# Kernel tuning notes

Measured on AMD Instinct MI355X. Metric: run time of the kernel, lower is better.

## Reference

```python
import jax, jax.numpy as jnp
import numpy as np

# dissected_Conv2d forward: grouped conv (groups=in_channels) producing one
# feature map per (input_channel, output_channel) pair, then permute_add_featuremaps:
# a gather by add_perm followed by a segmented sum over input channels, plus bias.

IN_C, OUT_C = 64, 64
KH, KW = 3, 3
B, H, W = 8, 56, 56
PAD = 1


def setup_inputs() -> dict:
    key = jax.random.key(0)
    k1, k2, k3 = jax.random.split(key, 3)
    x = jax.random.normal(k1, (B, IN_C, H, W), dtype=jnp.float32)
    # from_conv.weight: [out_channels, in_channels, kh, kw]
    weight = jax.random.normal(k2, (OUT_C, IN_C, KH, KW), dtype=jnp.float32) * 0.05
    bias = jax.random.normal(k3, (OUT_C,), dtype=jnp.float32) * 0.05
    return {"x": x, "weight": weight, "bias": bias}


def reference(x, weight, bias):
    out_c, in_c, kh, kw = weight.shape
    # make_preadd_conv: weight.view(in*out, 1, kh, kw)[weight_perm].
    # weight_perm maps grouped-conv channel k = i*out + j  ->  W[j, i], i.e. a
    # (out,in) -> (in,out) transpose of the leading dims.
    w_grp = jnp.transpose(weight, (1, 0, 2, 3)).reshape(in_c * out_c, 1, kh, kw)
    # grouped conv, groups = in_channels: group i convolves input channel i with
    # out_c kernels, giving preadd[:, i*out + j] = conv2d(x[:, i], W[j, i]).
    preadd = jax.lax.conv_general_dilated(
        x, w_grp,
        window_strides=(1, 1),
        padding=((PAD, PAD), (PAD, PAD)),
        dimension_numbers=("NCHW", "OIHW", "NCHW"),
        feature_group_count=in_c,
    )  # [B, in*out, H, W]
    # permute_add_featuremaps: gather with add_perm (channel p = o*in + i pulls
    # preadd channel i*out + o), then split/cat/sum == reshape [B,out,in,H,W].sum(in).
    p = jnp.arange(out_c * in_c)
    add_perm = (p % in_c) * out_c + p // in_c
    gathered = preadd[:, add_perm]  # [B, out*in, H, W]
    b_, _, h_, w_ = gathered.shape
    summed = gathered.reshape(b_, out_c, in_c, h_, w_).sum(axis=2)  # [B, out, H, W]
    # bias add: from_conv.bias.unsqueeze(1).unsqueeze(1) broadcast over H, W
    return summed + bias[None, :, None, None]
```

## Files before the change

kernel.cpp:

```cpp
#include <hip/hip_runtime.h>


typedef __attribute__((ext_vector_type(8))) short bf8_t;
typedef __attribute__((ext_vector_type(4))) float f4_t;

#define IC 64
#define OC 64
#define HH 56
#define WW 56
#define NB 8
#define NS 18
#define NPIX (HH * WW)
#define LCOLS 66
#define LDS_U16 (3 * LCOLS * 64)

__device__ __forceinline__ unsigned short f2bf(float f) {
    unsigned u = __float_as_uint(f);
    return (unsigned short)((u + 0x7FFFu + ((u >> 16) & 1u)) >> 16);
}

__global__ __launch_bounds__(256)
void repack_w(const float* __restrict__ w, unsigned short* __restrict__ wf) {
    const int s    = blockIdx.x;
    const int tid  = threadIdx.x;
    const int wv   = tid >> 6;
    const int lane = tid & 63;
    const int oc   = wv * 16 + (lane & 15);
    const int kg   = lane >> 4;
    const int tap  = s >> 1;
    const int ic0  = (s & 1) * 32 + kg * 8;
    unsigned short tmp[8];
    #pragma unroll
    for (int j = 0; j < 8; ++j)
        tmp[j] = f2bf(w[(oc * IC + ic0 + j) * 9 + tap]);
    *(uint4*)&wf[(((s * 4 + wv) * 64) + lane) * 8] = *(const uint4*)tmp;
}

__global__ __launch_bounds__(256)
void conv_fused(const float* __restrict__ x, const unsigned short* __restrict__ wf,
                const float* __restrict__ bias, float* __restrict__ out) {
    __shared__ unsigned short xl[LDS_U16];

    int bid = (int)blockIdx.x;
    bid = (bid & 7) * (NB * HH / 8) + (bid >> 3);
    const int b = bid / HH;
    const int h = bid - b * HH;

    const int tid  = threadIdx.x;
    const int wv   = tid >> 6;
    const int lane = tid & 63;
    const int kg   = lane >> 4;
    const int l15  = lane & 15;

    bf8_t afrag[NS];
    #pragma unroll
    for (int s = 0; s < NS; ++s)
        afrag[s] = *(const bf8_t*)&wf[(((s * 4 + wv) * 64) + lane) * 8];

    for (int i = tid; i < LDS_U16 / 8; i += 256)
        ((uint4*)xl)[i] = uint4{0u, 0u, 0u, 0u};
    __syncthreads();

    {
        const int ci  = lane - 1;
        const bool cok = (ci >= 0) && (ci < WW);
        #pragma unroll
        for (int i = 0; i < 6; ++i) {
            const int combo = wv + 4 * i;
            const int icb = combo / 3;
            const int r   = combo - icb * 3;
            const int hh  = h - 1 + r;
            if (cok && hh >= 0 && hh < HH) {
                const float* src = &x[((b * IC + icb * 8) * HH + hh) * WW + ci];
                bf8_t v;
                #pragma unroll
                for (int j = 0; j < 8; ++j)
                    v[j] = (short)f2bf(src[j * HH * WW]);
                const int W = r * LCOLS + lane;
                const unsigned byte = (unsigned)W * 128u +
                                      ((unsigned)(icb ^ (W & 7)) << 4);
                *(bf8_t*)((char*)xl + byte) = v;
            }
        }
    }
    __syncthreads();

    f4_t acc[4];
    #pragma unroll
    for (int t = 0; t < 4; ++t) acc[t] = 0.f;

    #pragma unroll
    for (int s = 0; s < NS; ++s) {
        const int tap = s >> 1;
        const int dh  = tap / 3;
        const int dw  = tap - dh * 3;
        const int c   = (s & 1) * 4 + kg;
        const int R0  = dh * LCOLS + dw + l15;
        const unsigned byte0 = (unsigned)R0 * 128u +
                               ((unsigned)(c ^ (R0 & 7)) << 4);
        const char* p = (const char*)xl + byte0;
        #pragma unroll
        for (int t = 0; t < 4; ++t) {
            const bf8_t bv = *(const bf8_t*)(p + t * 2048);
            acc[t] = __builtin_amdgcn_mfma_f32_16x16x32_bf16(afrag[s], bv, acc[t], 0, 0, 0);
        }
    }

    const int oc_c = wv * 16 + kg * 4;
    float bb[4];
    #pragma unroll
    for (int rr = 0; rr < 4; ++rr) bb[rr] = bias[oc_c + rr];
    #pragma unroll
    for (int t = 0; t < 4; ++t) {
        const int px = t * 16 + l15;
        if (px < WW) {
            float* o = &out[((b * OC + oc_c) * HH + h) * WW + px];
            #pragma unroll
            for (int rr = 0; rr < 4; ++rr)
                o[rr * HH * WW] = acc[t][rr] + bb[rr];
        }
    }
}

extern "C" void kernel_launch(void* const* d_in, const int* in_sizes, int n_in,
                              void* d_out, int out_size, void* d_ws, size_t ws_size,
                              hipStream_t stream) {
    const float* x    = (const float*)d_in[0];
    const float* w    = (const float*)d_in[1];
    const float* bias = (const float*)d_in[2];
    float* out        = (float*)d_out;

    unsigned short* wf = (unsigned short*)d_ws;

    hipLaunchKernelGGL(repack_w,  dim3(NS),      dim3(256), 0, stream, w, wf);
    hipLaunchKernelGGL(conv_fused, dim3(NB * HH), dim3(256), 0, stream,
                       x, wf, bias, out);
}
```

Baseline: 68.95 us.

## Split each output row into two half-row blocks and drop LDS zero-fill

```diff
diff --git a/kernel.cpp b/kernel.cpp
--- a/kernel.cpp
+++ b/kernel.cpp
@@ -11,8 +11,8 @@
 #define NB 8
 #define NS 18
 #define NPIX (HH * WW)
-#define LCOLS 66
-#define LDS_U16 (3 * LCOLS * 64)
+#define LC34 34
+#define LDS_U16 (3 * LC34 * 64)
 
 __device__ __forceinline__ unsigned short f2bf(float f) {
     unsigned u = __float_as_uint(f);
@@ -37,14 +37,16 @@
 }
 
 __global__ __launch_bounds__(256)
-void conv_fused(const float* __restrict__ x, const unsigned short* __restrict__ wf,
-                const float* __restrict__ bias, float* __restrict__ out) {
+void conv_half(const float* __restrict__ x, const unsigned short* __restrict__ wf,
+               const float* __restrict__ bias, float* __restrict__ out) {
     __shared__ unsigned short xl[LDS_U16];
 
     int bid = (int)blockIdx.x;
-    bid = (bid & 7) * (NB * HH / 8) + (bid >> 3);
-    const int b = bid / HH;
-    const int h = bid - b * HH;
+    bid = (bid & 7) * (NB * HH * 2 / 8) + (bid >> 3);
+    const int b   = bid / (HH * 2);
+    const int rem = bid - b * (HH * 2);
+    const int h   = rem >> 1;
+    const int ph  = rem & 1;
 
     const int tid  = threadIdx.x;
     const int wv   = tid >> 6;
@@ -57,68 +59,75 @@
     for (int s = 0; s < NS; ++s)
         afrag[s] = *(const bf8_t*)&wf[(((s * 4 + wv) * 64) + lane) * 8];
 
-    for (int i = tid; i < LDS_U16 / 8; i += 256)
-        ((uint4*)xl)[i] = uint4{0u, 0u, 0u, 0u};
-    __syncthreads();
+    const int half = lane >> 5;
+    const int lc   = lane & 31;
+    const int ci   = ph * 28 - 1 + lc;
+    const bool doW = (lc < 30);
+    const bool cok = doW && (ci >= 0) && (ci < WW);
 
-    {
-        const int ci  = lane - 1;
-        const bool cok = (ci >= 0) && (ci < WW);
+    float rv[3][8];
+    #pragma unroll
+    for (int i = 0; i < 3; ++i) {
+        const int c   = wv * 6 + 2 * i + half;
+        const int icb = c / 3;
+        const int r   = c - 3 * icb;
+        const int hh  = h - 1 + r;
+        const bool ok = cok && (hh >= 0) && (hh < HH);
+        const float* src = &x[((b * IC + icb * 8) * HH + hh) * WW + ci];
         #pragma unroll
-        for (int i = 0; i < 6; ++i) {
-            const int combo = wv + 4 * i;
-            const int icb = combo / 3;
-            const int r   = combo - icb * 3;
-            const int hh  = h - 1 + r;
-            if (cok && hh >= 0 && hh < HH) {
-                const float* src = &x[((b * IC + icb * 8) * HH + hh) * WW + ci];
-                bf8_t v;
-                #pragma unroll
-                for (int j = 0; j < 8; ++j)
-                    v[j] = (short)f2bf(src[j * HH * WW]);
-                const int W = r * LCOLS + lane;
-                const unsigned byte = (unsigned)W * 128u +
-                                      ((unsigned)(icb ^ (W & 7)) << 4);
-                *(bf8_t*)((char*)xl + byte) = v;
-            }
-        }
+        for (int j = 0; j < 8; ++j)
+            rv[i][j] = ok ? src[j * HH * WW] : 0.f;
+    }
+    #pragma unroll
+    for (int i = 0; i < 3; ++i) {
+        const int c   = wv * 6 + 2 * i + half;
+        const int icb = c / 3;
+        const int r   = c - 3 * icb;
+        bf8_t v;
+        #pragma unroll
+        for (int j = 0; j < 8; ++j) v[j] = (short)f2bf(rv[i][j]);
+        const int W = r * LC34 + lc;
+        const unsigned byte = (unsigned)W * 128u +
+                              ((unsigned)(icb ^ (W & 7)) << 4);
+        if (doW) *(bf8_t*)((char*)xl + byte) = v;
     }
     __syncthreads();
 
-    f4_t acc[4];
-    #pragma unroll
-    for (int t = 0; t < 4; ++t) acc[t] = 0.f;
-
+    f4_t acc0 = {0.f, 0.f, 0.f, 0.f};
+    f4_t acc1 = {0.f, 0.f, 0.f, 0.f};
     #pragma unroll
     for (int s = 0; s < NS; ++s) {
         const int tap = s >> 1;
         const int dh  = tap / 3;
         const int dw  = tap - dh * 3;
-        const int c   = (s & 1) * 4 + kg;
-        const int R0  = dh * LCOLS + dw + l15;
-        const unsigned byte0 = (unsigned)R0 * 128u +
-                               ((unsigned)(c ^ (R0 & 7)) << 4);
+        const int c16 = (s & 1) * 4 + kg;
+        const int W0  = dh * LC34 + dw + l15;
+        const unsigned byte0 = (unsigned)W0 * 128u +
+                               ((unsigned)(c16 ^ (W0 & 7)) << 4);
         const char* p = (const char*)xl + byte0;
-        #pragma unroll
-        for (int t = 0; t < 4; ++t) {
-            const bf8_t bv = *(const bf8_t*)(p + t * 2048);
-            acc[t] = __builtin_amdgcn_mfma_f32_16x16x32_bf16(afrag[s], bv, acc[t], 0, 0, 0);
-        }
+        const bf8_t bv0 = *(const bf8_t*)p;
+        const bf8_t bv1 = *(const bf8_t*)(p + 2048);
+        acc0 = __builtin_amdgcn_mfma_f32_16x16x32_bf16(afrag[s], bv0, acc0, 0, 0, 0);
+        acc1 = __builtin_amdgcn_mfma_f32_16x16x32_bf16(afrag[s], bv1, acc1, 0, 0, 0);
     }
 
     const int oc_c = wv * 16 + kg * 4;
     float bb[4];
     #pragma unroll
     for (int rr = 0; rr < 4; ++rr) bb[rr] = bias[oc_c + rr];
-    #pragma unroll
-    for (int t = 0; t < 4; ++t) {
-        const int px = t * 16 + l15;
-        if (px < WW) {
-            float* o = &out[((b * OC + oc_c) * HH + h) * WW + px];
-            #pragma unroll
-            for (int rr = 0; rr < 4; ++rr)
-                o[rr * HH * WW] = acc[t][rr] + bb[rr];
-        }
+    {
+        const int px = ph * 28 + l15;
+        float* o = &out[((b * OC + oc_c) * HH + h) * WW + px];
+        #pragma unroll
+        for (int rr = 0; rr < 4; ++rr)
+            o[rr * NPIX] = acc0[rr] + bb[rr];
+    }
+    if (l15 < 12) {
+        const int px = ph * 28 + 16 + l15;
+        float* o = &out[((b * OC + oc_c) * HH + h) * WW + px];
+        #pragma unroll
+        for (int rr = 0; rr < 4; ++rr)
+            o[rr * NPIX] = acc1[rr] + bb[rr];
     }
 }
 
@@ -132,7 +141,7 @@
 
     unsigned short* wf = (unsigned short*)d_ws;
 
-    hipLaunchKernelGGL(repack_w,  dim3(NS),      dim3(256), 0, stream, w, wf);
-    hipLaunchKernelGGL(conv_fused, dim3(NB * HH), dim3(256), 0, stream,
+    hipLaunchKernelGGL(repack_w,  dim3(NS),          dim3(256), 0, stream, w, wf);
+    hipLaunchKernelGGL(conv_half, dim3(NB * HH * 2), dim3(256), 0, stream,
                        x, wf, bias, out);
 }
```

Result: no change. 68.46 us (-0.7%).
